# Optimization experiments

Hardware: AMD Instinct MI355X
Metric: run time of the kernel (lower is better)

The kernel has to match this reference:

```python
import jax, jax.numpy as jnp
import numpy as np

BETA_MAX = 0.995
BETA_MIN = 0.05
EPI_AGE_PENALTY = 0.02
EPI_STRENGTH_BOOST = 0.5
EPI_STRENGTH_DECAY = 0.995
EPI_WRITE_ALPHA = 0.5
EVICT_AGE_BOOST = 0.05
EVICT_STR_PENALTY = 0.5
SLOT_TEMP = 50.0
SWITCH_TAU = 0.5

B, H, K, U, OBS, SSUM, PROJ = 2048, 256, 32, 128, 128, 128, 128


def setup_inputs() -> dict:
    key = jax.random.key(0)
    ks = jax.random.split(key, 20)
    def gl(k, shape, fan_in):
        return jax.random.normal(k, shape, jnp.float32) / np.sqrt(fan_in).astype(np.float32)
    inp = {}
    inp['h_prev'] = jax.random.normal(ks[0], (B, H), jnp.float32)
    inp['keys'] = jax.random.normal(ks[1], (B, K, H), jnp.float32)
    inp['vals'] = jax.random.normal(ks[2], (B, K, H), jnp.float32)
    inp['age'] = jax.random.uniform(ks[3], (B, K), jnp.float32) * 100.0
    inp['strength'] = jax.random.uniform(ks[4], (B, K), jnp.float32)
    inp['obs'] = jax.random.normal(ks[5], (B, OBS), jnp.float32)
    inp['ssum'] = jax.random.normal(ks[6], (B, SSUM), jnp.float32)
    inp['u_int_prev'] = jax.random.normal(ks[7], (B, U), jnp.float32)
    inp['step_in_macro'] = jax.random.randint(ks[8], (B,), 0, 4, jnp.int32)
    # learned parameters
    inp['W_obs'] = gl(ks[9], (OBS, PROJ), OBS); inp['b_obs'] = jnp.zeros((PROJ,), jnp.float32)
    inp['W_ssum'] = gl(ks[10], (SSUM, PROJ), SSUM); inp['b_ssum'] = jnp.zeros((PROJ,), jnp.float32)
    XIN = 2 * PROJ
    inp['Wi'] = gl(ks[11], (XIN, 3 * H), XIN); inp['bi'] = jnp.zeros((3 * H,), jnp.float32)
    inp['Wh'] = gl(ks[12], (H, 3 * H), H); inp['bhn'] = jnp.zeros((H,), jnp.float32)
    inp['W_gate'] = gl(ks[13], (H, 1), H); inp['b_gate'] = jnp.zeros((1,), jnp.float32)
    inp['W_mean'] = gl(ks[14], (2 * H, U), 2 * H); inp['b_mean'] = jnp.zeros((U,), jnp.float32)
    inp['u_logstd'] = jnp.full((U,), -1.0, jnp.float32)
    inp['W_beta'] = gl(ks[15], (2 * H, 1), 2 * H); inp['b_beta'] = jnp.zeros((1,), jnp.float32)
    inp['W_sw'] = gl(ks[16], (2 * H, 1), 2 * H); inp['b_sw'] = jnp.zeros((1,), jnp.float32)
    return inp


def reference(h_prev, keys, vals, age, strength, obs, ssum, u_int_prev, step_in_macro,
              W_obs, b_obs, W_ssum, b_ssum, Wi, bi, Wh, bhn, W_gate, b_gate,
              W_mean, b_mean, u_logstd, W_beta, b_beta, W_sw, b_sw):
    Kslots = keys.shape[1]
    # input projections + GRU step (flax GRUCell: h' = (1-z)*n + z*h)
    xo = jnp.tanh(obs @ W_obs + b_obs)
    xs = jnp.tanh(ssum @ W_ssum + b_ssum)
    x_in = jnp.concatenate([xo, xs], axis=-1)
    gi = x_in @ Wi + bi
    gh = h_prev @ Wh
    ir, iz, inn = jnp.split(gi, 3, axis=-1)
    hr, hz, hn = jnp.split(gh, 3, axis=-1)
    r = jax.nn.sigmoid(ir + hr)
    z = jax.nn.sigmoid(iz + hz)
    n = jnp.tanh(inn + r * (hn + bhn))
    h_t = (1.0 - z) * n + z * h_prev
    # write gate
    w_str = jax.nn.sigmoid(h_t @ W_gate + b_gate)  # [B,1]
    # episodic slot memory: cosine-sim read
    qn = h_t / (jnp.linalg.norm(h_t, axis=-1, keepdims=True) + 1e-6)
    kn = keys / (jnp.linalg.norm(keys, axis=-1, keepdims=True) + 1e-6)
    sim_r = jnp.einsum('bkd,bd->bk', kn, qn)
    logits = sim_r + EPI_STRENGTH_BOOST * jnp.log(jnp.clip(strength, 1e-3, 1.0)) - EPI_AGE_PENALTY * age
    w_read = jax.nn.softmax(logits, axis=-1)
    read_out = jnp.einsum('bk,bkd->bd', w_read, vals)
    # write addressing (write_vec == query_vec == h_t so sim_w == sim_r)
    wk_n = qn
    sim_w = sim_r
    evict = EVICT_AGE_BOOST * jnp.log1p(age) - EVICT_STR_PENALTY * strength
    write_soft = jax.nn.softmax(sim_w * SLOT_TEMP + evict, axis=-1)
    write_hard = jax.nn.one_hot(jnp.argmax(write_soft, axis=-1), Kslots, dtype=jnp.float32)
    write_w = jax.lax.stop_gradient(write_hard - write_soft) + write_soft  # straight-through
    ws = jnp.clip(w_str, 0.0, 1.0)  # [B,1]
    eff_rate = write_w * ws * EPI_WRITE_ALPHA  # [B,K]
    rate = eff_rate[:, :, None]
    keys_new = (1.0 - rate) * keys + rate * wk_n[:, None, :]
    vals_new = (1.0 - rate) * vals + rate * h_t[:, None, :]
    age_new = (age + 1.0) * (1.0 - write_w)
    str_new = strength * EPI_STRENGTH_DECAY
    str_new = jnp.clip(str_new + write_w * ws * (1.0 - str_new), 0.0, 1.0)
    # heads
    ctx = jnp.concatenate([h_t, read_out], axis=-1)
    mean = ctx @ W_mean + b_mean
    beta = BETA_MIN + (BETA_MAX - BETA_MIN) * jax.nn.sigmoid((ctx @ W_beta + b_beta)[:, 0])
    sw_prob = jax.nn.sigmoid((ctx @ W_sw + b_sw)[:, 0])
    # deterministic path (rng=None): u_prop = mean, threshold switch
    u_prop = mean
    switch_f = jnp.where(sw_prob > SWITCH_TAU, 1.0, 0.0)
    is_boundary = jnp.where(step_in_macro == 0, 1.0, 0.0)
    switch_f = jnp.maximum(switch_f, is_boundary)
    sw_f = switch_f[:, None]
    beta_eff = beta[:, None] * (1.0 - sw_f)
    u_int = beta_eff * u_int_prev + (1.0 - beta_eff) * u_prop
    return (h_t, keys_new, vals_new, age_new, str_new, u_prop,
            switch_f.astype(jnp.int32), u_int, beta, sw_prob)
```

## Files before the change

kernel.cpp:

```cpp
#include <hip/hip_runtime.h>
#include <math.h>

#define Bdim 2048
#define Hdim 256
#define KS 32
#define Udim 128
#define OBSD 128
#define PROJD 128
#define H3 768

__device__ __forceinline__ float sigm(float x){ return 1.0f/(1.0f+__expf(-x)); }

typedef float __attribute__((ext_vector_type(4))) f32x4;

__device__ __forceinline__ float4 ntload4(const float* p){
    f32x4 v = __builtin_nontemporal_load((const f32x4*)p);
    return make_float4(v.x, v.y, v.z, v.w);
}
__device__ __forceinline__ void ntstore4(float* p, float4 q){
    f32x4 v = {q.x, q.y, q.z, q.w};
    __builtin_nontemporal_store(v, (f32x4*)p);
}

__global__ __launch_bounds__(256) void kA1(
    const float* __restrict__ obs, const float* __restrict__ ssum,
    const float* __restrict__ W_obs, const float* __restrict__ b_obs,
    const float* __restrict__ W_ssum, const float* __restrict__ b_ssum,
    float* __restrict__ xin)
{
    __shared__ float s_in[2][8][128];
    const int t = threadIdx.x;
    const int r0 = blockIdx.x * 8;

    {
        int r = t >> 5, c4 = (t & 31) << 2;
        float4 v = *(const float4*)(obs + (size_t)(r0+r)*OBSD + c4);
        s_in[0][r][c4+0]=v.x; s_in[0][r][c4+1]=v.y; s_in[0][r][c4+2]=v.z; s_in[0][r][c4+3]=v.w;
        v = *(const float4*)(ssum + (size_t)(r0+r)*OBSD + c4);
        s_in[1][r][c4+0]=v.x; s_in[1][r][c4+1]=v.y; s_in[1][r][c4+2]=v.z; s_in[1][r][c4+3]=v.w;
    }
    __syncthreads();

    const int col = t & 127;
    const int src = t >> 7;
    const float* Wp = src ? W_ssum : W_obs;
    const float bb = src ? b_ssum[col] : b_obs[col];

    float acc[8] = {0,0,0,0,0,0,0,0};
    for (int i=0;i<128;i++){
        float w = Wp[i*PROJD + col];
        #pragma unroll
        for (int r=0;r<8;r++) acc[r] = fmaf(s_in[src][r][i], w, acc[r]);
    }
    #pragma unroll
    for (int r=0;r<8;r++)
        xin[(size_t)(r0+r)*256 + t] = tanhf(acc[r] + bb);
}

__global__ __launch_bounds__(256) void kG2(
    const float* __restrict__ xin, const float* __restrict__ hp,
    const float* __restrict__ Wi, const float* __restrict__ Wh,
    float* __restrict__ g)
{
    __shared__ float Xt[2][16][68];
    __shared__ float Wt[2][16][64];

    const int t = threadIdx.x;
    const int bx = blockIdx.x >> 4;
    const int by = blockIdx.x & 15;
    const int r0 = bx * 64;
    const int c0 = by * 64;

    const int kbeg = (c0 >= 768) ? 256 : 0;
    const int kend = (c0 >= 512 && c0 < 768) ? 256 : 512;
    const int nck  = (kend - kbeg) >> 4;

    const int sr  = t >> 2;
    const int sk4 = (t & 3) << 2;
    const size_t xbase = (size_t)(r0 + sr) * 256 + sk4;
    const int wk  = t >> 4;
    const int wc4 = (t & 15) << 2;
    const int cW  = (c0 < 512) ? c0 : (c0 - 256);

    const int rowA = (t & 15) << 2;
    const int colA = (t >> 4) << 2;

    float acc[4][4] = {{0.f}};
    float4 xr, wr;

    {
        const int k0 = kbeg;
        const float* xs = (k0 < 256) ? (xin + xbase + k0) : (hp + xbase + (k0 - 256));
        xr = *(const float4*)xs;
        const int k = k0 + wk;
        const float* wsrc = (k < 256) ? (Wi + (size_t)k*H3 + c0 + wc4)
                                      : (Wh + (size_t)(k-256)*H3 + cW + wc4);
        wr = *(const float4*)wsrc;
    }
    Xt[0][sk4+0][sr] = xr.x; Xt[0][sk4+1][sr] = xr.y;
    Xt[0][sk4+2][sr] = xr.z; Xt[0][sk4+3][sr] = xr.w;
    *(float4*)&Wt[0][wk][wc4] = wr;
    __syncthreads();

    for (int ck = 0; ck < nck; ck++){
        const int cur = ck & 1;
        const bool more = (ck + 1 < nck);
        if (more){
            const int k0 = kbeg + ((ck + 1) << 4);
            const float* xs = (k0 < 256) ? (xin + xbase + k0) : (hp + xbase + (k0 - 256));
            xr = *(const float4*)xs;
            const int k = k0 + wk;
            const float* wsrc = (k < 256) ? (Wi + (size_t)k*H3 + c0 + wc4)
                                          : (Wh + (size_t)(k-256)*H3 + cW + wc4);
            wr = *(const float4*)wsrc;
        }
        #pragma unroll
        for (int kk = 0; kk < 16; kk++){
            float4 a4 = *(const float4*)&Xt[cur][kk][rowA];
            float4 b4 = *(const float4*)&Wt[cur][kk][colA];
            float av[4] = {a4.x, a4.y, a4.z, a4.w};
            float bv[4] = {b4.x, b4.y, b4.z, b4.w};
            #pragma unroll
            for (int i=0;i<4;i++)
                #pragma unroll
                for (int j=0;j<4;j++)
                    acc[i][j] = fmaf(av[i], bv[j], acc[i][j]);
        }
        if (more){
            const int nxt = cur ^ 1;
            Xt[nxt][sk4+0][sr] = xr.x; Xt[nxt][sk4+1][sr] = xr.y;
            Xt[nxt][sk4+2][sr] = xr.z; Xt[nxt][sk4+3][sr] = xr.w;
            *(float4*)&Wt[nxt][wk][wc4] = wr;
            __syncthreads();
        }
    }

    #pragma unroll
    for (int i=0;i<4;i++){
        float4 o = make_float4(acc[i][0], acc[i][1], acc[i][2], acc[i][3]);
        *(float4*)&g[(size_t)(r0 + rowA + i)*1024 + c0 + colA] = o;
    }
}

__global__ __launch_bounds__(256) void kA3(
    const float* __restrict__ g, const float* __restrict__ h_prev,
    const float* __restrict__ bi, const float* __restrict__ bhn,
    const float* __restrict__ W_gate, const float* __restrict__ b_gate,
    float* __restrict__ out_h, float* __restrict__ ws_qn, float* __restrict__ ws_wstr)
{
    __shared__ float redA[8][4], redB[8][4];
    __shared__ float s_inv[8];
    const int t = threadIdx.x;
    const int r0 = blockIdx.x * 8;

    const float bir = bi[t], biz = bi[t+256], bin_ = bi[t+512];
    const float bh = bhn[t];
    const float wg = W_gate[t];
    const int lane = t & 63, wid = t >> 6;

    float hv[8];
    #pragma unroll
    for (int r=0;r<8;r++){
        const size_t gb = (size_t)(r0+r)*1024;
        float gr = g[gb + t];
        float gz = g[gb + 256 + t];
        float gni = g[gb + 512 + t];
        float gnh = g[gb + 768 + t];
        float hp = h_prev[(size_t)(r0+r)*Hdim + t];
        float rr = sigm(gr + bir);
        float zz = sigm(gz + biz);
        float nn = tanhf(gni + bin_ + rr*(gnh + bh));
        hv[r] = (1.0f - zz)*nn + zz*hp;
    }

    #pragma unroll
    for (int r=0;r<8;r++){
        float a = hv[r]*hv[r];
        float b2 = hv[r]*wg;
        #pragma unroll
        for (int off=32; off>=1; off>>=1){
            a  += __shfl_down(a, off);
            b2 += __shfl_down(b2, off);
        }
        if (lane==0){ redA[r][wid]=a; redB[r][wid]=b2; }
    }
    __syncthreads();
    if (t < 8){
        float ss = redA[t][0]+redA[t][1]+redA[t][2]+redA[t][3];
        float gd = redB[t][0]+redB[t][1]+redB[t][2]+redB[t][3];
        s_inv[t] = 1.0f/(sqrtf(ss) + 1e-6f);
        ws_wstr[r0+t] = sigm(gd + b_gate[0]);
    }
    __syncthreads();
    #pragma unroll
    for (int r=0;r<8;r++){
        out_h[(size_t)(r0+r)*Hdim + t] = hv[r];
        ws_qn[(size_t)(r0+r)*Hdim + t] = hv[r]*s_inv[r];
    }
}

__global__ __launch_bounds__(256) void kB(
    const float* __restrict__ keys, const float* __restrict__ vals,
    const float* __restrict__ age, const float* __restrict__ strength,
    const float* __restrict__ h_t, const float* __restrict__ ws_qn,
    const float* __restrict__ ws_wstr,
    float* __restrict__ keys_new, float* __restrict__ vals_new,
    float* __restrict__ age_new, float* __restrict__ str_new,
    float* __restrict__ ws_ro)
{
    __shared__ float s_sim[KS], s_wr[KS], s_rate[KS];
    __shared__ float4 s_ro[4][64];

    const int b = blockIdx.x;
    const int t = threadIdx.x, lane = t & 63, wid = t >> 6;

    float ag = 0.f, st = 0.f, wstr = 0.f;
    if (t < KS){
        ag = age[b*KS+t];
        st = strength[b*KS+t];
        wstr = ws_wstr[b];
    }

    const float4 q4 = ((const float4*)(ws_qn + (size_t)b*Hdim))[lane];
    const float4 h4 = ((const float4*)(h_t  + (size_t)b*Hdim))[lane];

    const float* Kb = keys + (size_t)b*KS*Hdim;
    const float* Vb = vals + (size_t)b*KS*Hdim;
    float4 kreg[8], vreg[8];
    float v[16];
    #pragma unroll
    for (int s=0;s<8;s++){
        const int k = wid*8 + s;
        kreg[s] = ntload4(Kb + k*Hdim + lane*4);
        vreg[s] = ntload4(Vb + k*Hdim + lane*4);
        v[2*s]   = kreg[s].x*q4.x + kreg[s].y*q4.y + kreg[s].z*q4.z + kreg[s].w*q4.w;
        v[2*s+1] = kreg[s].x*kreg[s].x + kreg[s].y*kreg[s].y + kreg[s].z*kreg[s].z + kreg[s].w*kreg[s].w;
    }

    {
        const bool hb5 = (lane & 32) != 0;
        #pragma unroll
        for (int i=0;i<8;i++){
            float send = hb5 ? v[i] : v[i+8];
            float recv = __shfl_xor(send, 32);
            v[i] = (hb5 ? v[i+8] : v[i]) + recv;
        }
        const bool hb4 = (lane & 16) != 0;
        #pragma unroll
        for (int i=0;i<4;i++){
            float send = hb4 ? v[i] : v[i+4];
            float recv = __shfl_xor(send, 16);
            v[i] = (hb4 ? v[i+4] : v[i]) + recv;
        }
        const bool hb3 = (lane & 8) != 0;
        #pragma unroll
        for (int i=0;i<2;i++){
            float send = hb3 ? v[i] : v[i+2];
            float recv = __shfl_xor(send, 8);
            v[i] = (hb3 ? v[i+2] : v[i]) + recv;
        }
        const bool hb2 = (lane & 4) != 0;
        {
            float send = hb2 ? v[0] : v[1];
            float recv = __shfl_xor(send, 4);
            v[0] = (hb2 ? v[1] : v[0]) + recv;
        }
        float r0 = v[0];
        r0 += __shfl_xor(r0, 2);
        r0 += __shfl_xor(r0, 1);
        float other = __shfl_xor(r0, 4);
        if ((lane & 7) == 0){
            s_sim[wid*8 + (lane>>3)] = r0 / (sqrtf(other) + 1e-6f);
        }
    }
    __syncthreads();

    if (t < KS){
        float sim = s_sim[t];
        float cl = fminf(fmaxf(st, 0.001f), 1.0f);
        float logit = sim + 0.5f*logf(cl) - 0.02f*ag;
        float wl = 50.0f*sim + 0.05f*log1pf(ag) - 0.5f*st;

        float lmax = logit;
        #pragma unroll
        for (int off=16; off>=1; off>>=1)
            lmax = fmaxf(lmax, __shfl_xor(lmax, off));
        float e = __expf(logit - lmax);
        float es = e;
        #pragma unroll
        for (int off=16; off>=1; off>>=1)
            es += __shfl_xor(es, off);

        float wm = wl; int ki = t;
        #pragma unroll
        for (int off=16; off>=1; off>>=1){
            float ow = __shfl_xor(wm, off);
            int   ok = __shfl_xor(ki, off);
            if (ow > wm || (ow == wm && ok < ki)){ wm = ow; ki = ok; }
        }

        s_wr[t] = e / es;
        float hard = (t == ki) ? 1.0f : 0.0f;
        s_rate[t] = hard * 0.5f * wstr;
        age_new[b*KS+t] = (ag + 1.0f)*(1.0f - hard);
        float sd = st*0.995f;
        float sn = sd + hard*wstr*(1.0f - sd);
        str_new[b*KS+t] = fminf(fmaxf(sn,0.f),1.f);
    }
    __syncthreads();

    float4 ro = make_float4(0.f,0.f,0.f,0.f);
    float* KNb = keys_new + (size_t)b*KS*Hdim;
    float* VNb = vals_new + (size_t)b*KS*Hdim;
    #pragma unroll
    for (int s=0;s<8;s++){
        const int k = wid*8 + s;
        const float wr = s_wr[k];
        const float rate = s_rate[k];
        const float om = 1.0f - rate;
        ro.x = fmaf(wr, vreg[s].x, ro.x);
        ro.y = fmaf(wr, vreg[s].y, ro.y);
        ro.z = fmaf(wr, vreg[s].z, ro.z);
        ro.w = fmaf(wr, vreg[s].w, ro.w);
        float4 kn, vn;
        kn.x = om*kreg[s].x + rate*q4.x;
        kn.y = om*kreg[s].y + rate*q4.y;
        kn.z = om*kreg[s].z + rate*q4.z;
        kn.w = om*kreg[s].w + rate*q4.w;
        vn.x = om*vreg[s].x + rate*h4.x;
        vn.y = om*vreg[s].y + rate*h4.y;
        vn.z = om*vreg[s].z + rate*h4.z;
        vn.w = om*vreg[s].w + rate*h4.w;
        ntstore4(KNb + k*Hdim + lane*4, kn);
        ntstore4(VNb + k*Hdim + lane*4, vn);
    }
    s_ro[wid][lane] = ro;
    __syncthreads();
    if (t < 64){
        float4 a = s_ro[0][t], bb = s_ro[1][t], c = s_ro[2][t], d = s_ro[3][t];
        float4 r;
        r.x = a.x+bb.x+c.x+d.x;
        r.y = a.y+bb.y+c.y+d.y;
        r.z = a.z+bb.z+c.z+d.z;
        r.w = a.w+bb.w+c.w+d.w;
        ((float4*)(ws_ro + (size_t)b*Hdim))[t] = r;
    }
}

__global__ __launch_bounds__(256) void kC(
    const float* __restrict__ h_t, const float* __restrict__ ws_ro,
    const float* __restrict__ u_int_prev, const int* __restrict__ step_in_macro,
    const float* __restrict__ W_mean, const float* __restrict__ b_mean,
    const float* __restrict__ W_beta, const float* __restrict__ b_beta,
    const float* __restrict__ W_sw, const float* __restrict__ b_sw,
    float* __restrict__ out_uprop, float* __restrict__ out_switch,
    float* __restrict__ out_uint, float* __restrict__ out_beta, float* __restrict__ out_swp)
{
    __shared__ float s_ctx[4][512];
    __shared__ float redb[4][4], reds[4][4];
    __shared__ float s_beff[4];
    const int t = threadIdx.x;
    const int r0 = blockIdx.x * 4;

    {
        int r = t >> 6, c4 = (t & 63) << 2;
        float4 v = *(const float4*)(h_t + (size_t)(r0+r)*Hdim + c4);
        s_ctx[r][c4+0]=v.x; s_ctx[r][c4+1]=v.y; s_ctx[r][c4+2]=v.z; s_ctx[r][c4+3]=v.w;
        v = *(const float4*)(ws_ro + (size_t)(r0+r)*Hdim + c4);
        s_ctx[r][256+c4+0]=v.x; s_ctx[r][256+c4+1]=v.y; s_ctx[r][256+c4+2]=v.z; s_ctx[r][256+c4+3]=v.w;
    }
    __syncthreads();

    const int c = t & 127;
    const int rh = t >> 7;
    float acc[2] = {0.f, 0.f};
    for (int i=0;i<512;i++){
        float w = W_mean[i*Udim + c];
        acc[0] = fmaf(s_ctx[2*rh+0][i], w, acc[0]);
        acc[1] = fmaf(s_ctx[2*rh+1][i], w, acc[1]);
    }

    float pb[4]={0,0,0,0}, ps[4]={0,0,0,0};
    for (int i=t; i<512; i+=256){
        float wb = W_beta[i], wsw = W_sw[i];
        #pragma unroll
        for (int r=0;r<4;r++){
            pb[r] = fmaf(s_ctx[r][i], wb, pb[r]);
            ps[r] = fmaf(s_ctx[r][i], wsw, ps[r]);
        }
    }
    const int lane = t & 63, wid = t >> 6;
    #pragma unroll
    for (int r=0;r<4;r++){
        float a = pb[r], b2 = ps[r];
        #pragma unroll
        for (int off=32; off>=1; off>>=1){
            a  += __shfl_down(a, off);
            b2 += __shfl_down(b2, off);
        }
        if (lane==0){ redb[r][wid]=a; reds[r][wid]=b2; }
    }
    __syncthreads();
    if (t < 4){
        float db  = redb[t][0]+redb[t][1]+redb[t][2]+redb[t][3] + b_beta[0];
        float dsw = reds[t][0]+reds[t][1]+reds[t][2]+reds[t][3] + b_sw[0];
        float beta = 0.05f + 0.945f*sigm(db);
        float swp = sigm(dsw);
        float swf = (swp > 0.5f) ? 1.0f : 0.0f;
        if (step_in_macro[r0+t] == 0) swf = 1.0f;
        out_beta[r0+t] = beta;
        out_swp[r0+t] = swp;
        out_switch[r0+t] = swf;
        s_beff[t] = beta*(1.0f - swf);
    }
    __syncthreads();
    #pragma unroll
    for (int j=0;j<2;j++){
        int r = 2*rh + j;
        float mean = acc[j] + b_mean[c];
        size_t o = (size_t)(r0+r)*Udim + c;
        out_uprop[o] = mean;
        float be = s_beff[r];
        out_uint[o] = be*u_int_prev[o] + (1.0f-be)*mean;
    }
}

extern "C" void kernel_launch(void* const* d_in, const int* in_sizes, int n_in,
                              void* d_out, int out_size, void* d_ws, size_t ws_size,
                              hipStream_t stream)
{
    const float* h_prev   = (const float*)d_in[0];
    const float* keys     = (const float*)d_in[1];
    const float* vals     = (const float*)d_in[2];
    const float* age      = (const float*)d_in[3];
    const float* strength = (const float*)d_in[4];
    const float* obs      = (const float*)d_in[5];
    const float* ssum     = (const float*)d_in[6];
    const float* u_int_prev = (const float*)d_in[7];
    const int*   step     = (const int*)d_in[8];
    const float* W_obs    = (const float*)d_in[9];
    const float* b_obs    = (const float*)d_in[10];
    const float* W_ssum   = (const float*)d_in[11];
    const float* b_ssum   = (const float*)d_in[12];
    const float* Wi       = (const float*)d_in[13];
    const float* bi       = (const float*)d_in[14];
    const float* Wh       = (const float*)d_in[15];
    const float* bhn      = (const float*)d_in[16];
    const float* W_gate   = (const float*)d_in[17];
    const float* b_gate   = (const float*)d_in[18];
    const float* W_mean   = (const float*)d_in[19];
    const float* b_mean   = (const float*)d_in[20];
    const float* W_beta   = (const float*)d_in[22];
    const float* b_beta   = (const float*)d_in[23];
    const float* W_sw     = (const float*)d_in[24];
    const float* b_sw     = (const float*)d_in[25];

    float* out = (float*)d_out;
    float* out_h    = out;
    float* out_kn   = out_h   + 524288;
    float* out_vn   = out_kn  + 16777216;
    float* out_age  = out_vn  + 16777216;
    float* out_str  = out_age + 65536;
    float* out_up   = out_str + 65536;
    float* out_sw   = out_up  + 262144;
    float* out_ui   = out_sw  + 2048;
    float* out_beta = out_ui  + 262144;
    float* out_swp  = out_beta+ 2048;

    float* ws = (float*)d_ws;
    float* ws_qn   = ws;
    float* ws_ro   = ws + Bdim*Hdim;
    float* ws_wstr = ws + 2*Bdim*Hdim;

    float* ws_xin = out_vn;
    float* ws_g   = out_kn;

    kA1<<<Bdim/8, 256, 0, stream>>>(obs, ssum, W_obs, b_obs, W_ssum, b_ssum, ws_xin);
    kG2<<<512, 256, 0, stream>>>(ws_xin, h_prev, Wi, Wh, ws_g);
    kA3<<<Bdim/8, 256, 0, stream>>>(ws_g, h_prev, bi, bhn, W_gate, b_gate,
                                    out_h, ws_qn, ws_wstr);
    kB<<<Bdim, 256, 0, stream>>>(keys, vals, age, strength, out_h, ws_qn, ws_wstr,
                                 out_kn, out_vn, out_age, out_str, ws_ro);
    kC<<<Bdim/4, 256, 0, stream>>>(out_h, ws_ro, u_int_prev, step, W_mean, b_mean,
                                   W_beta, b_beta, W_sw, b_sw,
                                   out_up, out_sw, out_ui, out_beta, out_swp);
}
```

Baseline: 126.9 us.

## Halve rows per block in small kernels, deepen GEMM k-tile, shuffle softmax weights

kA1 and kA3 now process 4 rows per block instead of 8, doubling the grid to 512 blocks so more CUs are busy. The kG2 GEMM k-chunk grows from 16 to 32, halving the number of barrier-separated iterations at the cost of twice the shared memory and more staging registers. kB has every wave redundantly compute the slot softmax and argmax in its own lanes, then broadcasts the weights with __shfl instead of going through shared memory. This removes one __syncthreads per batch row in exchange for duplicated transcendental work in four waves.

```diff
diff --git a/kernel.cpp b/kernel.cpp
--- a/kernel.cpp
+++ b/kernel.cpp
@@ -28,16 +28,16 @@
     const float* __restrict__ W_ssum, const float* __restrict__ b_ssum,
     float* __restrict__ xin)
 {
-    __shared__ float s_in[2][8][128];
+    __shared__ float s_in[2][4][128];
     const int t = threadIdx.x;
-    const int r0 = blockIdx.x * 8;
+    const int r0 = blockIdx.x * 4;
 
     {
-        int r = t >> 5, c4 = (t & 31) << 2;
-        float4 v = *(const float4*)(obs + (size_t)(r0+r)*OBSD + c4);
-        s_in[0][r][c4+0]=v.x; s_in[0][r][c4+1]=v.y; s_in[0][r][c4+2]=v.z; s_in[0][r][c4+3]=v.w;
-        v = *(const float4*)(ssum + (size_t)(r0+r)*OBSD + c4);
-        s_in[1][r][c4+0]=v.x; s_in[1][r][c4+1]=v.y; s_in[1][r][c4+2]=v.z; s_in[1][r][c4+3]=v.w;
+        int src = t >> 7, r = (t >> 5) & 3, c4 = (t & 31) << 2;
+        const float* base = src ? ssum : obs;
+        float4 v = *(const float4*)(base + (size_t)(r0+r)*OBSD + c4);
+        s_in[src][r][c4+0]=v.x; s_in[src][r][c4+1]=v.y;
+        s_in[src][r][c4+2]=v.z; s_in[src][r][c4+3]=v.w;
     }
     __syncthreads();
 
@@ -46,14 +46,14 @@
     const float* Wp = src ? W_ssum : W_obs;
     const float bb = src ? b_ssum[col] : b_obs[col];
 
-    float acc[8] = {0,0,0,0,0,0,0,0};
+    float acc[4] = {0,0,0,0};
     for (int i=0;i<128;i++){
         float w = Wp[i*PROJD + col];
         #pragma unroll
-        for (int r=0;r<8;r++) acc[r] = fmaf(s_in[src][r][i], w, acc[r]);
-    }
-    #pragma unroll
-    for (int r=0;r<8;r++)
+        for (int r=0;r<4;r++) acc[r] = fmaf(s_in[src][r][i], w, acc[r]);
+    }
+    #pragma unroll
+    for (int r=0;r<4;r++)
         xin[(size_t)(r0+r)*256 + t] = tanhf(acc[r] + bb);
 }
 
@@ -62,8 +62,8 @@
     const float* __restrict__ Wi, const float* __restrict__ Wh,
     float* __restrict__ g)
 {
-    __shared__ float Xt[2][16][68];
-    __shared__ float Wt[2][16][64];
+    __shared__ float Xt[2][32][68];
+    __shared__ float Wt[2][32][64];
 
     const int t = threadIdx.x;
     const int bx = blockIdx.x >> 4;
@@ -73,49 +73,52 @@
 
     const int kbeg = (c0 >= 768) ? 256 : 0;
     const int kend = (c0 >= 512 && c0 < 768) ? 256 : 512;
-    const int nck  = (kend - kbeg) >> 4;
-
-    const int sr  = t >> 2;
-    const int sk4 = (t & 3) << 2;
-    const size_t xbase = (size_t)(r0 + sr) * 256 + sk4;
-    const int wk  = t >> 4;
-    const int wc4 = (t & 15) << 2;
+    const int nck  = (kend - kbeg) >> 5;
+
     const int cW  = (c0 < 512) ? c0 : (c0 - 256);
-
     const int rowA = (t & 15) << 2;
     const int colA = (t >> 4) << 2;
 
+    const int xrow0 = (2*t+0) >> 3, xk40 = ((2*t+0) & 7) << 2;
+    const int xrow1 = (2*t+1) >> 3, xk41 = ((2*t+1) & 7) << 2;
+    const int wk0 = (2*t+0) >> 4, wc40 = ((2*t+0) & 15) << 2;
+    const int wk1 = (2*t+1) >> 4, wc41 = ((2*t+1) & 15) << 2;
+
     float acc[4][4] = {{0.f}};
-    float4 xr, wr;
+    float4 xr0, xr1, wr0, wr1;
+
+    #define LOADX(row, k4, k0) \
+        ( ((k0)+(k4)) < 256 ? *(const float4*)(xin + (size_t)(r0+(row))*256 + (k0)+(k4)) \
+                            : *(const float4*)(hp  + (size_t)(r0+(row))*256 + (k0)+(k4)-256) )
+    #define LOADW(wk, wc4, k0) \
+        ( ((k0)+(wk)) < 256 ? *(const float4*)(Wi + (size_t)((k0)+(wk))*H3 + c0 + (wc4)) \
+                            : *(const float4*)(Wh + (size_t)((k0)+(wk)-256)*H3 + cW + (wc4)) )
 
     {
         const int k0 = kbeg;
-        const float* xs = (k0 < 256) ? (xin + xbase + k0) : (hp + xbase + (k0 - 256));
-        xr = *(const float4*)xs;
-        const int k = k0 + wk;
-        const float* wsrc = (k < 256) ? (Wi + (size_t)k*H3 + c0 + wc4)
-                                      : (Wh + (size_t)(k-256)*H3 + cW + wc4);
-        wr = *(const float4*)wsrc;
-    }
-    Xt[0][sk4+0][sr] = xr.x; Xt[0][sk4+1][sr] = xr.y;
-    Xt[0][sk4+2][sr] = xr.z; Xt[0][sk4+3][sr] = xr.w;
-    *(float4*)&Wt[0][wk][wc4] = wr;
+        xr0 = LOADX(xrow0, xk40, k0);
+        xr1 = LOADX(xrow1, xk41, k0);
+        wr0 = LOADW(wk0, wc40, k0);
+        wr1 = LOADW(wk1, wc41, k0);
+    }
+    Xt[0][xk40+0][xrow0]=xr0.x; Xt[0][xk40+1][xrow0]=xr0.y; Xt[0][xk40+2][xrow0]=xr0.z; Xt[0][xk40+3][xrow0]=xr0.w;
+    Xt[0][xk41+0][xrow1]=xr1.x; Xt[0][xk41+1][xrow1]=xr1.y; Xt[0][xk41+2][xrow1]=xr1.z; Xt[0][xk41+3][xrow1]=xr1.w;
+    *(float4*)&Wt[0][wk0][wc40] = wr0;
+    *(float4*)&Wt[0][wk1][wc41] = wr1;
     __syncthreads();
 
     for (int ck = 0; ck < nck; ck++){
         const int cur = ck & 1;
         const bool more = (ck + 1 < nck);
         if (more){
-            const int k0 = kbeg + ((ck + 1) << 4);
-            const float* xs = (k0 < 256) ? (xin + xbase + k0) : (hp + xbase + (k0 - 256));
-            xr = *(const float4*)xs;
-            const int k = k0 + wk;
-            const float* wsrc = (k < 256) ? (Wi + (size_t)k*H3 + c0 + wc4)
-                                          : (Wh + (size_t)(k-256)*H3 + cW + wc4);
-            wr = *(const float4*)wsrc;
-        }
-        #pragma unroll
-        for (int kk = 0; kk < 16; kk++){
+            const int k0 = kbeg + ((ck + 1) << 5);
+            xr0 = LOADX(xrow0, xk40, k0);
+            xr1 = LOADX(xrow1, xk41, k0);
+            wr0 = LOADW(wk0, wc40, k0);
+            wr1 = LOADW(wk1, wc41, k0);
+        }
+        #pragma unroll
+        for (int kk = 0; kk < 32; kk++){
             float4 a4 = *(const float4*)&Xt[cur][kk][rowA];
             float4 b4 = *(const float4*)&Wt[cur][kk][colA];
             float av[4] = {a4.x, a4.y, a4.z, a4.w};
@@ -128,12 +131,15 @@
         }
         if (more){
             const int nxt = cur ^ 1;
-            Xt[nxt][sk4+0][sr] = xr.x; Xt[nxt][sk4+1][sr] = xr.y;
-            Xt[nxt][sk4+2][sr] = xr.z; Xt[nxt][sk4+3][sr] = xr.w;
-            *(float4*)&Wt[nxt][wk][wc4] = wr;
+            Xt[nxt][xk40+0][xrow0]=xr0.x; Xt[nxt][xk40+1][xrow0]=xr0.y; Xt[nxt][xk40+2][xrow0]=xr0.z; Xt[nxt][xk40+3][xrow0]=xr0.w;
+            Xt[nxt][xk41+0][xrow1]=xr1.x; Xt[nxt][xk41+1][xrow1]=xr1.y; Xt[nxt][xk41+2][xrow1]=xr1.z; Xt[nxt][xk41+3][xrow1]=xr1.w;
+            *(float4*)&Wt[nxt][wk0][wc40] = wr0;
+            *(float4*)&Wt[nxt][wk1][wc41] = wr1;
             __syncthreads();
         }
     }
+    #undef LOADX
+    #undef LOADW
 
     #pragma unroll
     for (int i=0;i<4;i++){
@@ -148,19 +154,19 @@
     const float* __restrict__ W_gate, const float* __restrict__ b_gate,
     float* __restrict__ out_h, float* __restrict__ ws_qn, float* __restrict__ ws_wstr)
 {
-    __shared__ float redA[8][4], redB[8][4];
-    __shared__ float s_inv[8];
+    __shared__ float redA[4][4], redB[4][4];
+    __shared__ float s_inv[4];
     const int t = threadIdx.x;
-    const int r0 = blockIdx.x * 8;
+    const int r0 = blockIdx.x * 4;
 
     const float bir = bi[t], biz = bi[t+256], bin_ = bi[t+512];
     const float bh = bhn[t];
     const float wg = W_gate[t];
     const int lane = t & 63, wid = t >> 6;
 
-    float hv[8];
-    #pragma unroll
-    for (int r=0;r<8;r++){
+    float hv[4];
+    #pragma unroll
+    for (int r=0;r<4;r++){
         const size_t gb = (size_t)(r0+r)*1024;
         float gr = g[gb + t];
         float gz = g[gb + 256 + t];
@@ -174,7 +180,7 @@
     }
 
     #pragma unroll
-    for (int r=0;r<8;r++){
+    for (int r=0;r<4;r++){
         float a = hv[r]*hv[r];
         float b2 = hv[r]*wg;
         #pragma unroll
@@ -185,7 +191,7 @@
         if (lane==0){ redA[r][wid]=a; redB[r][wid]=b2; }
     }
     __syncthreads();
-    if (t < 8){
+    if (t < 4){
         float ss = redA[t][0]+redA[t][1]+redA[t][2]+redA[t][3];
         float gd = redB[t][0]+redB[t][1]+redB[t][2]+redB[t][3];
         s_inv[t] = 1.0f/(sqrtf(ss) + 1e-6f);
@@ -193,7 +199,7 @@
     }
     __syncthreads();
     #pragma unroll
-    for (int r=0;r<8;r++){
+    for (int r=0;r<4;r++){
         out_h[(size_t)(r0+r)*Hdim + t] = hv[r];
         ws_qn[(size_t)(r0+r)*Hdim + t] = hv[r]*s_inv[r];
     }
@@ -208,18 +214,15 @@
     float* __restrict__ age_new, float* __restrict__ str_new,
     float* __restrict__ ws_ro)
 {
-    __shared__ float s_sim[KS], s_wr[KS], s_rate[KS];
+    __shared__ float s_sim[KS];
     __shared__ float4 s_ro[4][64];
 
     const int b = blockIdx.x;
     const int t = threadIdx.x, lane = t & 63, wid = t >> 6;
 
-    float ag = 0.f, st = 0.f, wstr = 0.f;
-    if (t < KS){
-        ag = age[b*KS+t];
-        st = strength[b*KS+t];
-        wstr = ws_wstr[b];
-    }
+    const float ag = age[b*KS + (lane & 31)];
+    const float st = strength[b*KS + (lane & 31)];
+    const float wstr = ws_wstr[b];
 
     const float4 q4 = ((const float4*)(ws_qn + (size_t)b*Hdim))[lane];
     const float4 h4 = ((const float4*)(h_t  + (size_t)b*Hdim))[lane];
@@ -275,8 +278,10 @@
     }
     __syncthreads();
 
-    if (t < KS){
-        float sim = s_sim[t];
+    float wr_l, rate_l;
+    {
+        const int sl = lane & 31;
+        float sim = s_sim[sl];
         float cl = fminf(fmaxf(st, 0.001f), 1.0f);
         float logit = sim + 0.5f*logf(cl) - 0.02f*ag;
         float wl = 50.0f*sim + 0.05f*log1pf(ag) - 0.5f*st;
@@ -291,7 +296,7 @@
         for (int off=16; off>=1; off>>=1)
             es += __shfl_xor(es, off);
 
-        float wm = wl; int ki = t;
+        float wm = wl; int ki = sl;
         #pragma unroll
         for (int off=16; off>=1; off>>=1){
             float ow = __shfl_xor(wm, off);
@@ -299,15 +304,17 @@
             if (ow > wm || (ow == wm && ok < ki)){ wm = ow; ki = ok; }
         }
 
-        s_wr[t] = e / es;
-        float hard = (t == ki) ? 1.0f : 0.0f;
-        s_rate[t] = hard * 0.5f * wstr;
-        age_new[b*KS+t] = (ag + 1.0f)*(1.0f - hard);
-        float sd = st*0.995f;
-        float sn = sd + hard*wstr*(1.0f - sd);
-        str_new[b*KS+t] = fminf(fmaxf(sn,0.f),1.f);
-    }
-    __syncthreads();
+        wr_l = e / es;
+        float hard = (sl == ki) ? 1.0f : 0.0f;
+        rate_l = hard * 0.5f * wstr;
+
+        if (wid == 0 && lane < KS){
+            age_new[b*KS+lane] = (ag + 1.0f)*(1.0f - hard);
+            float sd = st*0.995f;
+            float sn = sd + hard*wstr*(1.0f - sd);
+            str_new[b*KS+lane] = fminf(fmaxf(sn,0.f),1.f);
+        }
+    }
 
     float4 ro = make_float4(0.f,0.f,0.f,0.f);
     float* KNb = keys_new + (size_t)b*KS*Hdim;
@@ -315,8 +322,8 @@
     #pragma unroll
     for (int s=0;s<8;s++){
         const int k = wid*8 + s;
-        const float wr = s_wr[k];
-        const float rate = s_rate[k];
+        const float wr = __shfl(wr_l, k);
+        const float rate = __shfl(rate_l, k);
         const float om = 1.0f - rate;
         ro.x = fmaf(wr, vreg[s].x, ro.x);
         ro.y = fmaf(wr, vreg[s].y, ro.y);
@@ -475,9 +482,9 @@
     float* ws_xin = out_vn;
     float* ws_g   = out_kn;
 
-    kA1<<<Bdim/8, 256, 0, stream>>>(obs, ssum, W_obs, b_obs, W_ssum, b_ssum, ws_xin);
+    kA1<<<Bdim/4, 256, 0, stream>>>(obs, ssum, W_obs, b_obs, W_ssum, b_ssum, ws_xin);
     kG2<<<512, 256, 0, stream>>>(ws_xin, h_prev, Wi, Wh, ws_g);
-    kA3<<<Bdim/8, 256, 0, stream>>>(ws_g, h_prev, bi, bhn, W_gate, b_gate,
+    kA3<<<Bdim/4, 256, 0, stream>>>(ws_g, h_prev, bi, bhn, W_gate, b_gate,
                                     out_h, ws_qn, ws_wstr);
     kB<<<Bdim, 256, 0, stream>>>(keys, vals, age, strength, out_h, ws_qn, ws_wstr,
                                  out_kn, out_vn, out_age, out_str, ws_ro);
```

After: 138.1 us. 8.8% more time.
